# Performance work log

Hardware: AMD Instinct MI355X
Metric: run time of the kernel (lower is better)

Reference implementation:

```python
import jax, jax.numpy as jnp
import numpy as np

D_MSA = 256
D_PAIR = 128
N_HEADS = 8
HEAD_DIM = D_MSA // N_HEADS
EPS = 1e-5


def setup_inputs() -> dict:
    key = jax.random.key(0)
    ks = jax.random.split(key, 14)
    s = 0.02
    return {
        "msa": jax.random.normal(ks[0], (1, 64, 256, D_MSA), dtype=jnp.float32),
        "pair": jax.random.normal(ks[1], (1, 256, 256, D_PAIR), dtype=jnp.float32),
        "Wq": jax.random.normal(ks[2], (D_MSA, D_MSA), dtype=jnp.float32) * s,
        "bq": jnp.zeros((D_MSA,), jnp.float32),
        "Wk": jax.random.normal(ks[3], (D_MSA, D_MSA), dtype=jnp.float32) * s,
        "bk": jnp.zeros((D_MSA,), jnp.float32),
        "Wv": jax.random.normal(ks[4], (D_MSA, D_MSA), dtype=jnp.float32) * s,
        "bv": jnp.zeros((D_MSA,), jnp.float32),
        "Wpb": jax.random.normal(ks[5], (D_PAIR, N_HEADS), dtype=jnp.float32) * s,
        "bpb": jnp.zeros((N_HEADS,), jnp.float32),
        "Wo": jax.random.normal(ks[6], (D_MSA, D_MSA), dtype=jnp.float32) * s,
        "bo": jnp.zeros((D_MSA,), jnp.float32),
        "gamma": jnp.ones((D_MSA,), jnp.float32),
        "beta": jnp.zeros((D_MSA,), jnp.float32),
    }


def reference(msa, pair, Wq, bq, Wk, bk, Wv, bv, Wpb, bpb, Wo, bo, gamma, beta):
    B, N, L, D = msa.shape
    H, Hd = N_HEADS, HEAD_DIM
    # projections -> (B, N, L, H, Hd)
    q = (msa @ Wq + bq).reshape(B, N, L, H, Hd)
    k = (msa @ Wk + bk).reshape(B, N, L, H, Hd)
    v = (msa @ Wv + bv).reshape(B, N, L, H, Hd)
    # scores: (B, N, H, L, L)
    scores = jnp.einsum('bnihd,bnjhd->bnhij', q, k) / jnp.sqrt(jnp.float32(Hd))
    # pair bias: (B, L, L, H) -> (B, H, L, L), broadcast over N
    pb = jnp.transpose(pair @ Wpb + bpb, (0, 3, 1, 2))
    scores = scores + pb[:, None]
    attn = jax.nn.softmax(scores, axis=-1)
    attn_out = jnp.einsum('bnhij,bnjhd->bnihd', attn, v).reshape(B, N, L, D)
    attn_out = attn_out @ Wo + bo
    # residual + LayerNorm
    x = msa + attn_out
    mu = jnp.mean(x, axis=-1, keepdims=True)
    var = jnp.var(x, axis=-1, keepdims=True)
    return (x - mu) * jax.lax.rsqrt(var + EPS) * gamma + beta
```

## Files before the change

kernel.cpp:

```cpp
#include <hip/hip_runtime.h>

#define NSEQ 64
#define LL   256
#define DD   256
#define HH   8
#define HDIM 32

typedef short short8  __attribute__((ext_vector_type(8)));
typedef short short4v __attribute__((ext_vector_type(4)));
typedef float float4v __attribute__((ext_vector_type(4)));

#define MFMA16(a,b,c) __builtin_amdgcn_mfma_f32_16x16x32_bf16((a),(b),(c),0,0,0)

__device__ __forceinline__ float4v zero4() {
  float4v z;
  z[0] = 0.f; z[1] = 0.f; z[2] = 0.f; z[3] = 0.f;
  return z;
}

__device__ __forceinline__ short f2b(float f) {
  unsigned u = __float_as_uint(f);
  u = (u + 0x7fffu + ((u >> 16) & 1u)) >> 16;
  return (short)u;
}

__device__ __forceinline__ float b2f(short s) {
  return __uint_as_float(((unsigned)(unsigned short)s) << 16);
}

__device__ __forceinline__ short8 cvt8(const float* p) {
  float4 a = *(const float4*)p;
  float4 b = *(const float4*)(p + 4);
  short8 r;
  r[0] = f2b(a.x); r[1] = f2b(a.y); r[2] = f2b(a.z); r[3] = f2b(a.w);
  r[4] = f2b(b.x); r[5] = f2b(b.y); r[6] = f2b(b.z); r[7] = f2b(b.w);
  return r;
}

__device__ __forceinline__ void ld_lds16(const void* g, void* l) {
  __builtin_amdgcn_global_load_lds(
      (const __attribute__((address_space(1))) unsigned int*)g,
      (__attribute__((address_space(3))) unsigned int*)l, 16, 0, 0);
}
#define WAIT_VM0() __builtin_amdgcn_s_waitcnt(0x0F70)

#define WT_OFF    0
#define PB_OFF    (4*65536*2)
#define PBF_OFF   (PB_OFF + 8*65536*2)
#define Q_OFF     (PB_OFF + 8*65536*4)
#define K_OFF     (Q_OFF  + 16384*256*2)
#define VT_OFF    (K_OFF  + 16384*256*2)
#define MSA16_OFF (VT_OFF + 16384*256*2)
#define O_OFF     MSA16_OFF

__global__ __launch_bounds__(256) void k1_prep(
    const float* __restrict__ msa,  const float* __restrict__ pair,
    const float* __restrict__ Wq,   const float* __restrict__ Wk,
    const float* __restrict__ Wv,   const float* __restrict__ Wpb,
    const float* __restrict__ bpb,  const float* __restrict__ Wo,
    char* __restrict__ ws)
{
  __shared__ short ldsWt[16 * 136];
  int bx = blockIdx.x, tid = threadIdx.x;
  if (bx < 256) {
    short* pb16 = (short*)(ws + PB_OFF);
    for (int i = tid; i < 16 * 136; i += 256) ldsWt[i] = 0;
    __syncthreads();
    {
      float4 wv4 = *(const float4*)&Wpb[tid * 4];
      int kk = (tid * 4) >> 3, n0 = (tid * 4) & 7;
      ldsWt[(n0 + 0) * 136 + kk] = f2b(wv4.x);
      ldsWt[(n0 + 1) * 136 + kk] = f2b(wv4.y);
      ldsWt[(n0 + 2) * 136 + kk] = f2b(wv4.z);
      ldsWt[(n0 + 3) * 136 + kk] = f2b(wv4.w);
    }
    __syncthreads();
    int w = tid >> 6, l = tid & 63, q = l >> 4, c = l & 15;
    int base = bx * 256 + w * 64;
    float bias = bpb[c & 7];
    short8 bf[4];
#pragma unroll
    for (int ks = 0; ks < 4; ks++)
      bf[ks] = *(const short8*)&ldsWt[c * 136 + ks * 32 + q * 8];
    float4v acc[4];
#pragma unroll
    for (int mt = 0; mt < 4; mt++) acc[mt] = zero4();
#pragma unroll
    for (int ks = 0; ks < 4; ks++) {
#pragma unroll
      for (int mt = 0; mt < 4; mt++) {
        short8 af = cvt8(&pair[(base + mt * 16 + c) * 128 + ks * 32 + q * 8]);
        acc[mt] = MFMA16(af, bf[ks], acc[mt]);
      }
    }
    if (c < 8) {
#pragma unroll
      for (int mt = 0; mt < 4; mt++) {
        short4v o;
#pragma unroll
        for (int r = 0; r < 4; r++) o[r] = f2b(acc[mt][r] + bias);
        *(short4v*)&pb16[c * 65536 + base + mt * 16 + q * 4] = o;
      }
    }
  } else if (bx < 1280) {
    int b2 = bx - 256;
    int mat = b2 >> 8, r = b2 & 255;
    const float* W = (mat == 0) ? Wq : (mat == 1) ? Wk : (mat == 2) ? Wv : Wo;
    short* wt = (short*)(ws + WT_OFF) + mat * 65536;
    wt[tid * 256 + r] = f2b(W[r * 256 + tid]);
  } else {
    int b3 = bx - 1280;
    const float* src = msa + b3 * 8192;
    short* dst = (short*)(ws + MSA16_OFF) + b3 * 8192;
#pragma unroll
    for (int i = 0; i < 8; i++) {
      int idx = i * 1024 + tid * 4;
      float4 v = *(const float4*)&src[idx];
      short4v s;
      s[0] = f2b(v.x); s[1] = f2b(v.y); s[2] = f2b(v.z); s[3] = f2b(v.w);
      *(short4v*)&dst[idx] = s;
    }
  }
}

__global__ __launch_bounds__(256) void k2_qkv(
    const float* __restrict__ bq, const float* __restrict__ bk,
    const float* __restrict__ bv, char* __restrict__ ws)
{
  __shared__ __align__(16) short lsA[128 * 128];
  __shared__ __align__(16) short lsB[128 * 128];
  int bx = blockIdx.x, tid = threadIdx.x;
  if (bx >= 768) {
    int b = bx - 768;
    int it16 = b & 15;
    const short* src = (const short*)(ws + PB_OFF) + (b >> 4) * 65536 + it16 * 4096;
    short* pbf = (short*)(ws + PBF_OFF);
    short* lt = lsA;
#pragma unroll
    for (int i2 = 0; i2 < 2; i2++) {
      int idx = i2 * 2048 + tid * 8;
      *(short8*)&lt[(idx >> 8) * 264 + (idx & 255)] = *(const short8*)&src[idx];
    }
    __syncthreads();
#pragma unroll
    for (int i2 = 0; i2 < 4; i2++) {
      int fid = i2 * 256 + tid;
      int jt = fid >> 6, lane = fid & 63;
      int qp = lane >> 4, cp = lane & 15;
      short4v v;
#pragma unroll
      for (int r = 0; r < 4; r++)
        v[r] = lt[(qp * 4 + r) * 264 + jt * 16 + cp];
      *(short4v*)&pbf[((b * 16 + jt) * 64 + lane) * 4] = v;
    }
    return;
  }
  int rt = bx & 127, ct = bx >> 7;
  int m = ct >> 1, cb = (ct & 1) * 128;
  int R0 = rt * 128;
  const short* msa16 = (const short*)(ws + MSA16_OFF);
  const short* wt = (const short*)(ws + WT_OFF) + m * 65536;
  int w = tid >> 6, l = tid & 63, q = l >> 4, c = l & 15;
  int WR = (w & 1) * 64, WC = (w >> 1) * 64;
  float4v acc[4][4];
#pragma unroll
  for (int mt = 0; mt < 4; mt++)
#pragma unroll
    for (int nt = 0; nt < 4; nt++) acc[mt][nt] = zero4();

#pragma unroll 1
  for (int kk = 0; kk < 2; kk++) {
    if (kk) __syncthreads();
#pragma unroll
    for (int i = 0; i < 8; i++) {
      int ci = i * 256 + tid;
      int r = ci >> 4, pos = ci & 15;
      int kc = pos ^ (r & 7);
      ld_lds16(&msa16[(R0 + r) * 256 + kk * 128 + kc * 8], &lsA[ci * 8]);
    }
#pragma unroll
    for (int i = 0; i < 8; i++) {
      int ci = i * 256 + tid;
      int r = ci >> 4, pos = ci & 15;
      int kc = pos ^ (r & 7);
      ld_lds16(&wt[(cb + r) * 256 + kk * 128 + kc * 8], &lsB[ci * 8]);
    }
    WAIT_VM0();
    __syncthreads();
#pragma unroll
    for (int ks = 0; ks < 4; ks++) {
      short8 af[4], bf[4];
#pragma unroll
      for (int mt = 0; mt < 4; mt++) {
        int r = WR + mt * 16 + c;
        int phys = (ks * 4 + q) ^ (r & 7);
        af[mt] = *(const short8*)&lsA[r * 128 + phys * 8];
      }
#pragma unroll
      for (int nt = 0; nt < 4; nt++) {
        int r = WC + nt * 16 + c;
        int phys = (ks * 4 + q) ^ (r & 7);
        bf[nt] = *(const short8*)&lsB[r * 128 + phys * 8];
      }
#pragma unroll
      for (int mt = 0; mt < 4; mt++)
#pragma unroll
        for (int nt = 0; nt < 4; nt++)
          acc[mt][nt] = MFMA16(af[mt], bf[nt], acc[mt][nt]);
    }
  }

  const float* bp = (m == 0) ? bq : (m == 1) ? bk : bv;
  int n = R0 >> 8;
  if (m < 2) {
    short* dst = (short*)(ws + (m == 0 ? Q_OFF : K_OFF));
#pragma unroll
    for (int nt = 0; nt < 4; nt++) {
      int ch = cb + WC + nt * 16 + c;
      float bb = bp[ch];
      int h = ch >> 5, hd = ch & 31;
#pragma unroll
      for (int mt = 0; mt < 4; mt++) {
        int i0 = (R0 & 255) + WR + mt * 16 + q * 4;
#pragma unroll
        for (int r = 0; r < 4; r++)
          dst[((n * HH + h) * 256 + i0 + r) * HDIM + hd] = f2b(acc[mt][nt][r] + bb);
      }
    }
  } else {
    short* vt = (short*)(ws + VT_OFF);
#pragma unroll
    for (int nt = 0; nt < 4; nt++) {
      int ch = cb + WC + nt * 16 + c;
      float bb = bp[ch];
#pragma unroll
      for (int mt = 0; mt < 4; mt++) {
        int j0 = (R0 & 255) + WR + mt * 16 + q * 4;
        short4v s4;
#pragma unroll
        for (int r = 0; r < 4; r++) s4[r] = f2b(acc[mt][nt][r] + bb);
        *(short4v*)&vt[((n * HH + (ch >> 5)) * HDIM + (ch & 31)) * 256 + j0] = s4;
      }
    }
  }
}

__global__ __launch_bounds__(256) void k3_attn(char* __restrict__ ws)
{
  __shared__ short P[64 * 264];
  int bx = blockIdx.x, tid = threadIdx.x;
  int qq = bx >> 9, grp = bx & 511;
  int n = grp >> 3, h = grp & 7;
  int w = tid >> 6, l = tid & 63, q = l >> 4, c = l & 15;
  const short* qh = (const short*)(ws + Q_OFF) + (n * HH + h) * 256 * HDIM;
  const short* kh = (const short*)(ws + K_OFF) + (n * HH + h) * 256 * HDIM;
  const short* vt = (const short*)(ws + VT_OFF) + (n * HH + h) * HDIM * 256;
  const short* pbf = (const short*)(ws + PBF_OFF) + (h * 16 + qq * 4 + w) * 16 * 256;
  short* os = (short*)(ws + O_OFF);
  const float scale = 0.17677669529663687f;
  int i0 = qq * 64 + w * 16;
  short8 aq = *(const short8*)&qh[(i0 + c) * HDIM + q * 8];
  float4v s[16];
#pragma unroll
  for (int jt = 0; jt < 16; jt++) {
    short8 bk8 = *(const short8*)&kh[(jt * 16 + c) * HDIM + q * 8];
    s[jt] = MFMA16(aq, bk8, zero4());
  }
#pragma unroll
  for (int jt = 0; jt < 16; jt++) {
    short4v pv = *(const short4v*)&pbf[(jt * 64 + l) * 4];
#pragma unroll
    for (int r = 0; r < 4; r++)
      s[jt][r] = __builtin_fmaf(s[jt][r], scale, b2f(pv[r]));
  }
  float inv[4];
#pragma unroll
  for (int r = 0; r < 4; r++) {
    float m = s[0][r];
#pragma unroll
    for (int jt = 1; jt < 16; jt++) m = fmaxf(m, s[jt][r]);
    m = fmaxf(m, __shfl_xor(m, 1, 64));
    m = fmaxf(m, __shfl_xor(m, 2, 64));
    m = fmaxf(m, __shfl_xor(m, 4, 64));
    m = fmaxf(m, __shfl_xor(m, 8, 64));
    float rs = 0.f;
#pragma unroll
    for (int jt = 0; jt < 16; jt++) {
      float p = __expf(s[jt][r] - m);
      s[jt][r] = p;
      rs += p;
    }
    rs += __shfl_xor(rs, 1, 64);
    rs += __shfl_xor(rs, 2, 64);
    rs += __shfl_xor(rs, 4, 64);
    rs += __shfl_xor(rs, 8, 64);
    inv[r] = 1.f / rs;
  }
#pragma unroll
  for (int jt = 0; jt < 16; jt++)
#pragma unroll
    for (int r = 0; r < 4; r++)
      P[(w * 16 + q * 4 + r) * 264 + jt * 16 + c] = f2b(s[jt][r]);
  float4v o0 = zero4(), o1 = zero4();
#pragma unroll
  for (int kk = 0; kk < 8; kk++) {
    short8 ap = *(const short8*)&P[(w * 16 + c) * 264 + kk * 32 + q * 8];
    short8 b0 = *(const short8*)&vt[c * 256 + kk * 32 + q * 8];
    short8 b1 = *(const short8*)&vt[(16 + c) * 256 + kk * 32 + q * 8];
    o0 = MFMA16(ap, b0, o0);
    o1 = MFMA16(ap, b1, o1);
  }
#pragma unroll
  for (int r = 0; r < 4; r++) {
    os[(n * 256 + i0 + q * 4 + r) * 256 + h * 32 + c]      = f2b(o0[r] * inv[r]);
    os[(n * 256 + i0 + q * 4 + r) * 256 + h * 32 + 16 + c] = f2b(o1[r] * inv[r]);
  }
}

__global__ __launch_bounds__(256) void k4_out(
    const float* __restrict__ msa, const float* __restrict__ bo,
    const float* __restrict__ gamma, const float* __restrict__ beta,
    const char* __restrict__ ws, float* __restrict__ out)
{
  __shared__ __align__(16) short lsA[64 * 128];
  __shared__ __align__(16) short lsB[256 * 128];
  int bx = blockIdx.x, tid = threadIdx.x;
  int w = tid >> 6, l = tid & 63, q = l >> 4, c = l & 15;
  int R0 = bx * 64;
  const short* osrc = (const short*)(ws + O_OFF);
  const short* wto  = (const short*)(ws + WT_OFF) + 3 * 65536;
  float4v acc[16];
#pragma unroll
  for (int nt = 0; nt < 16; nt++) acc[nt] = zero4();

#pragma unroll 1
  for (int kk = 0; kk < 2; kk++) {
    if (kk) __syncthreads();
#pragma unroll
    for (int i = 0; i < 4; i++) {
      int ci = i * 256 + tid;
      int r = ci >> 4, pos = ci & 15;
      int kc = pos ^ (r & 7);
      ld_lds16(&osrc[(R0 + r) * 256 + kk * 128 + kc * 8], &lsA[ci * 8]);
    }
#pragma unroll
    for (int i = 0; i < 16; i++) {
      int ci = i * 256 + tid;
      int r = ci >> 4, pos = ci & 15;
      int kc = pos ^ (r & 7);
      ld_lds16(&wto[r * 256 + kk * 128 + kc * 8], &lsB[ci * 8]);
    }
    WAIT_VM0();
    __syncthreads();
#pragma unroll
    for (int ks = 0; ks < 4; ks++) {
      int rA = w * 16 + c;
      int physA = (ks * 4 + q) ^ (rA & 7);
      short8 af = *(const short8*)&lsA[rA * 128 + physA * 8];
#pragma unroll
      for (int nt = 0; nt < 16; nt++) {
        int r = nt * 16 + c;
        int phys = (ks * 4 + q) ^ (r & 7);
        short8 bf = *(const short8*)&lsB[r * 128 + phys * 8];
        acc[nt] = MFMA16(af, bf, acc[nt]);
      }
    }
  }

  int r0 = R0 + w * 16;
  float s1[4] = {0, 0, 0, 0}, s2[4] = {0, 0, 0, 0};
#pragma unroll
  for (int nt = 0; nt < 16; nt++) {
    float bb = bo[nt * 16 + c];
#pragma unroll
    for (int r = 0; r < 4; r++) {
      float x = acc[nt][r] + bb + msa[(r0 + q * 4 + r) * 256 + nt * 16 + c];
      acc[nt][r] = x;
      s1[r] += x;
      s2[r] = __builtin_fmaf(x, x, s2[r]);
    }
  }
  float mu[4], rsd[4];
#pragma unroll
  for (int r = 0; r < 4; r++) {
    float a = s1[r], b = s2[r];
    a += __shfl_xor(a, 1, 64); b += __shfl_xor(b, 1, 64);
    a += __shfl_xor(a, 2, 64); b += __shfl_xor(b, 2, 64);
    a += __shfl_xor(a, 4, 64); b += __shfl_xor(b, 4, 64);
    a += __shfl_xor(a, 8, 64); b += __shfl_xor(b, 8, 64);
    float m = a * (1.f / 256.f);
    float v = __builtin_fmaf(-m, m, b * (1.f / 256.f));
    mu[r] = m;
    rsd[r] = rsqrtf(v + 1e-5f);
  }
#pragma unroll
  for (int nt = 0; nt < 16; nt++) {
    float g = gamma[nt * 16 + c], bt = beta[nt * 16 + c];
#pragma unroll
    for (int r = 0; r < 4; r++)
      out[(r0 + q * 4 + r) * 256 + nt * 16 + c] =
          (acc[nt][r] - mu[r]) * rsd[r] * g + bt;
  }
}

extern "C" void kernel_launch(void* const* d_in, const int* in_sizes, int n_in,
                              void* d_out, int out_size, void* d_ws, size_t ws_size,
                              hipStream_t stream)
{
  const float* msa   = (const float*)d_in[0];
  const float* pair  = (const float*)d_in[1];
  const float* Wq    = (const float*)d_in[2];
  const float* bq    = (const float*)d_in[3];
  const float* Wk    = (const float*)d_in[4];
  const float* bk    = (const float*)d_in[5];
  const float* Wv    = (const float*)d_in[6];
  const float* bv    = (const float*)d_in[7];
  const float* Wpb   = (const float*)d_in[8];
  const float* bpb   = (const float*)d_in[9];
  const float* Wo    = (const float*)d_in[10];
  const float* bo    = (const float*)d_in[11];
  const float* gamma = (const float*)d_in[12];
  const float* beta  = (const float*)d_in[13];
  char* ws = (char*)d_ws;
  float* out = (float*)d_out;

  hipLaunchKernelGGL(k1_prep, dim3(1792), dim3(256), 0, stream,
                     msa, pair, Wq, Wk, Wv, Wpb, bpb, Wo, ws);
  hipLaunchKernelGGL(k2_qkv, dim3(896), dim3(256), 0, stream,
                     bq, bk, bv, ws);
  hipLaunchKernelGGL(k3_attn, dim3(2048), dim3(256), 0, stream, ws);
  hipLaunchKernelGGL(k4_out, dim3(256), dim3(256), 0, stream,
                     msa, bo, gamma, beta, ws, out);
}
```

Baseline: 179.4 us.

## Spread pair-bias, weight transpose and output projection across more blocks

The pair-bias projection now uses 1024 blocks, each handling 64 rows instead of 256. The weight transpose now reads coalesced float4 tiles and transposes them through LDS, replacing the strided per-element stores. The output projection with LayerNorm now runs 16 rows per block across 1024 blocks. Each wave computes a 64-column slice straight from global memory, and row statistics are combined through a small LDS buffer. This raises occupancy and parallelism, but it gives up the LDS staging and reuse of Wo and adds a block-wide barrier.

```diff
diff --git a/kernel.cpp b/kernel.cpp
--- a/kernel.cpp
+++ b/kernel.cpp
@@ -60,56 +60,42 @@
     const float* __restrict__ bpb,  const float* __restrict__ Wo,
     char* __restrict__ ws)
 {
-  __shared__ short ldsWt[16 * 136];
+  __shared__ short lds[32 * 264];
   int bx = blockIdx.x, tid = threadIdx.x;
-  if (bx < 256) {
+  if (bx < 1024) {
     short* pb16 = (short*)(ws + PB_OFF);
-    for (int i = tid; i < 16 * 136; i += 256) ldsWt[i] = 0;
+    for (int i = tid; i < 16 * 136; i += 256) lds[i] = 0;
     __syncthreads();
     {
       float4 wv4 = *(const float4*)&Wpb[tid * 4];
       int kk = (tid * 4) >> 3, n0 = (tid * 4) & 7;
-      ldsWt[(n0 + 0) * 136 + kk] = f2b(wv4.x);
-      ldsWt[(n0 + 1) * 136 + kk] = f2b(wv4.y);
-      ldsWt[(n0 + 2) * 136 + kk] = f2b(wv4.z);
-      ldsWt[(n0 + 3) * 136 + kk] = f2b(wv4.w);
+      lds[(n0 + 0) * 136 + kk] = f2b(wv4.x);
+      lds[(n0 + 1) * 136 + kk] = f2b(wv4.y);
+      lds[(n0 + 2) * 136 + kk] = f2b(wv4.z);
+      lds[(n0 + 3) * 136 + kk] = f2b(wv4.w);
     }
     __syncthreads();
     int w = tid >> 6, l = tid & 63, q = l >> 4, c = l & 15;
-    int base = bx * 256 + w * 64;
-    float bias = bpb[c & 7];
-    short8 bf[4];
+    int base = bx * 64 + w * 16;
+    short8 bf[4], af[4];
 #pragma unroll
     for (int ks = 0; ks < 4; ks++)
-      bf[ks] = *(const short8*)&ldsWt[c * 136 + ks * 32 + q * 8];
-    float4v acc[4];
-#pragma unroll
-    for (int mt = 0; mt < 4; mt++) acc[mt] = zero4();
-#pragma unroll
-    for (int ks = 0; ks < 4; ks++) {
-#pragma unroll
-      for (int mt = 0; mt < 4; mt++) {
-        short8 af = cvt8(&pair[(base + mt * 16 + c) * 128 + ks * 32 + q * 8]);
-        acc[mt] = MFMA16(af, bf[ks], acc[mt]);
-      }
-    }
+      bf[ks] = *(const short8*)&lds[c * 136 + ks * 32 + q * 8];
+#pragma unroll
+    for (int ks = 0; ks < 4; ks++)
+      af[ks] = cvt8(&pair[(base + c) * 128 + ks * 32 + q * 8]);
+    float4v acc = zero4();
+#pragma unroll
+    for (int ks = 0; ks < 4; ks++) acc = MFMA16(af[ks], bf[ks], acc);
     if (c < 8) {
-#pragma unroll
-      for (int mt = 0; mt < 4; mt++) {
-        short4v o;
-#pragma unroll
-        for (int r = 0; r < 4; r++) o[r] = f2b(acc[mt][r] + bias);
-        *(short4v*)&pb16[c * 65536 + base + mt * 16 + q * 4] = o;
-      }
-    }
-  } else if (bx < 1280) {
-    int b2 = bx - 256;
-    int mat = b2 >> 8, r = b2 & 255;
-    const float* W = (mat == 0) ? Wq : (mat == 1) ? Wk : (mat == 2) ? Wv : Wo;
-    short* wt = (short*)(ws + WT_OFF) + mat * 65536;
-    wt[tid * 256 + r] = f2b(W[r * 256 + tid]);
-  } else {
-    int b3 = bx - 1280;
+      float bias = bpb[c];
+      short4v o;
+#pragma unroll
+      for (int r = 0; r < 4; r++) o[r] = f2b(acc[r] + bias);
+      *(short4v*)&pb16[c * 65536 + base + q * 4] = o;
+    }
+  } else if (bx < 1536) {
+    int b3 = bx - 1024;
     const float* src = msa + b3 * 8192;
     short* dst = (short*)(ws + MSA16_OFF) + b3 * 8192;
 #pragma unroll
@@ -119,6 +105,29 @@
       short4v s;
       s[0] = f2b(v.x); s[1] = f2b(v.y); s[2] = f2b(v.z); s[3] = f2b(v.w);
       *(short4v*)&dst[idx] = s;
+    }
+  } else {
+    int b2 = bx - 1536;
+    int mat = b2 >> 3, kt = b2 & 7;
+    const float* W = (mat == 0) ? Wq : (mat == 1) ? Wk : (mat == 2) ? Wv : Wo;
+    short* wt = (short*)(ws + WT_OFF) + mat * 65536;
+#pragma unroll
+    for (int i = 0; i < 8; i++) {
+      int idx = i * 1024 + tid * 4;
+      int k = idx >> 8, n = idx & 255;
+      float4 v = *(const float4*)&W[(kt * 32 + k) * 256 + n];
+      short4v s;
+      s[0] = f2b(v.x); s[1] = f2b(v.y); s[2] = f2b(v.z); s[3] = f2b(v.w);
+      *(short4v*)&lds[k * 264 + n] = s;
+    }
+    __syncthreads();
+    int n = tid;
+#pragma unroll
+    for (int g = 0; g < 4; g++) {
+      short8 o;
+#pragma unroll
+      for (int j = 0; j < 8; j++) o[j] = lds[(g * 8 + j) * 264 + n];
+      *(short8*)&wt[n * 256 + kt * 32 + g * 8] = o;
     }
   }
 }
@@ -322,65 +331,40 @@
     const float* __restrict__ gamma, const float* __restrict__ beta,
     const char* __restrict__ ws, float* __restrict__ out)
 {
-  __shared__ __align__(16) short lsA[64 * 128];
-  __shared__ __align__(16) short lsB[256 * 128];
+  __shared__ float lnbuf[2][4][16];
   int bx = blockIdx.x, tid = threadIdx.x;
   int w = tid >> 6, l = tid & 63, q = l >> 4, c = l & 15;
-  int R0 = bx * 64;
+  int R0 = bx * 16;
   const short* osrc = (const short*)(ws + O_OFF);
   const short* wto  = (const short*)(ws + WT_OFF) + 3 * 65536;
-  float4v acc[16];
-#pragma unroll
-  for (int nt = 0; nt < 16; nt++) acc[nt] = zero4();
-
-#pragma unroll 1
-  for (int kk = 0; kk < 2; kk++) {
-    if (kk) __syncthreads();
-#pragma unroll
-    for (int i = 0; i < 4; i++) {
-      int ci = i * 256 + tid;
-      int r = ci >> 4, pos = ci & 15;
-      int kc = pos ^ (r & 7);
-      ld_lds16(&osrc[(R0 + r) * 256 + kk * 128 + kc * 8], &lsA[ci * 8]);
-    }
-#pragma unroll
-    for (int i = 0; i < 16; i++) {
-      int ci = i * 256 + tid;
-      int r = ci >> 4, pos = ci & 15;
-      int kc = pos ^ (r & 7);
-      ld_lds16(&wto[r * 256 + kk * 128 + kc * 8], &lsB[ci * 8]);
-    }
-    WAIT_VM0();
-    __syncthreads();
-#pragma unroll
-    for (int ks = 0; ks < 4; ks++) {
-      int rA = w * 16 + c;
-      int physA = (ks * 4 + q) ^ (rA & 7);
-      short8 af = *(const short8*)&lsA[rA * 128 + physA * 8];
-#pragma unroll
-      for (int nt = 0; nt < 16; nt++) {
-        int r = nt * 16 + c;
-        int phys = (ks * 4 + q) ^ (r & 7);
-        short8 bf = *(const short8*)&lsB[r * 128 + phys * 8];
-        acc[nt] = MFMA16(af, bf, acc[nt]);
-      }
-    }
-  }
-
-  int r0 = R0 + w * 16;
+  short8 af[8];
+#pragma unroll
+  for (int ks = 0; ks < 8; ks++)
+    af[ks] = *(const short8*)&osrc[(R0 + c) * 256 + ks * 32 + q * 8];
+  float4v acc[4];
+#pragma unroll
+  for (int nt = 0; nt < 4; nt++) acc[nt] = zero4();
+#pragma unroll
+  for (int ks = 0; ks < 8; ks++) {
+#pragma unroll
+    for (int nt = 0; nt < 4; nt++) {
+      short8 bf = *(const short8*)&wto[(w * 64 + nt * 16 + c) * 256 + ks * 32 + q * 8];
+      acc[nt] = MFMA16(af[ks], bf, acc[nt]);
+    }
+  }
   float s1[4] = {0, 0, 0, 0}, s2[4] = {0, 0, 0, 0};
 #pragma unroll
-  for (int nt = 0; nt < 16; nt++) {
-    float bb = bo[nt * 16 + c];
+  for (int nt = 0; nt < 4; nt++) {
+    int col = w * 64 + nt * 16 + c;
+    float bb = bo[col];
 #pragma unroll
     for (int r = 0; r < 4; r++) {
-      float x = acc[nt][r] + bb + msa[(r0 + q * 4 + r) * 256 + nt * 16 + c];
+      float x = acc[nt][r] + bb + msa[(R0 + q * 4 + r) * 256 + col];
       acc[nt][r] = x;
       s1[r] += x;
       s2[r] = __builtin_fmaf(x, x, s2[r]);
     }
   }
-  float mu[4], rsd[4];
 #pragma unroll
   for (int r = 0; r < 4; r++) {
     float a = s1[r], b = s2[r];
@@ -388,17 +372,30 @@
     a += __shfl_xor(a, 2, 64); b += __shfl_xor(b, 2, 64);
     a += __shfl_xor(a, 4, 64); b += __shfl_xor(b, 4, 64);
     a += __shfl_xor(a, 8, 64); b += __shfl_xor(b, 8, 64);
+    if (c == 0) {
+      lnbuf[0][w][q * 4 + r] = a;
+      lnbuf[1][w][q * 4 + r] = b;
+    }
+  }
+  __syncthreads();
+  float mu[4], rsd[4];
+#pragma unroll
+  for (int r = 0; r < 4; r++) {
+    int row = q * 4 + r;
+    float a = lnbuf[0][0][row] + lnbuf[0][1][row] + lnbuf[0][2][row] + lnbuf[0][3][row];
+    float b = lnbuf[1][0][row] + lnbuf[1][1][row] + lnbuf[1][2][row] + lnbuf[1][3][row];
     float m = a * (1.f / 256.f);
     float v = __builtin_fmaf(-m, m, b * (1.f / 256.f));
     mu[r] = m;
     rsd[r] = rsqrtf(v + 1e-5f);
   }
 #pragma unroll
-  for (int nt = 0; nt < 16; nt++) {
-    float g = gamma[nt * 16 + c], bt = beta[nt * 16 + c];
+  for (int nt = 0; nt < 4; nt++) {
+    int col = w * 64 + nt * 16 + c;
+    float g = gamma[col], bt = beta[col];
 #pragma unroll
     for (int r = 0; r < 4; r++)
-      out[(r0 + q * 4 + r) * 256 + nt * 16 + c] =
+      out[(R0 + q * 4 + r) * 256 + col] =
           (acc[nt][r] - mu[r]) * rsd[r] * g + bt;
   }
 }
@@ -424,11 +421,11 @@
   char* ws = (char*)d_ws;
   float* out = (float*)d_out;
 
-  hipLaunchKernelGGL(k1_prep, dim3(1792), dim3(256), 0, stream,
+  hipLaunchKernelGGL(k1_prep, dim3(1568), dim3(256), 0, stream,
                      msa, pair, Wq, Wk, Wv, Wpb, bpb, Wo, ws);
   hipLaunchKernelGGL(k2_qkv, dim3(896), dim3(256), 0, stream,
                      bq, bk, bv, ws);
   hipLaunchKernelGGL(k3_attn, dim3(2048), dim3(256), 0, stream, ws);
-  hipLaunchKernelGGL(k4_out, dim3(256), dim3(256), 0, stream,
+  hipLaunchKernelGGL(k4_out, dim3(1024), dim3(256), 0, stream,
                      msa, bo, gamma, beta, ws, out);
 }
```

Measured after the change: 182.0 us. Within noise of the previous version (+1.5%).
